# Kernel tuning notes

Measured on AMD Instinct MI355X. Metric: run time of the kernel, lower is better.

The kernel has to match this reference:

```python
import jax, jax.numpy as jnp
import numpy as np

INPUT_DIM = 256
RNN_DIM = 256
T, B = 1024, 64


def setup_inputs() -> dict:
    key = jax.random.key(0)
    ks = jax.random.split(key, 12)
    stdv = 1.0 / np.sqrt(RNN_DIM)
    u = lambda k, shape: jax.random.uniform(k, shape, jnp.float32, -stdv, stdv)
    return {
        "input_vectors": jax.random.normal(ks[0], (T, B, INPUT_DIM), jnp.float32),
        "W": u(ks[1], (INPUT_DIM, RNN_DIM)),
        "U": u(ks[2], (RNN_DIM, RNN_DIM)),
        "b": u(ks[3], (1, RNN_DIM)),
        "W_r": u(ks[4], (INPUT_DIM, RNN_DIM)),
        "U_r": u(ks[5], (RNN_DIM, RNN_DIM)),
        "b_r": u(ks[6], (1, RNN_DIM)),
        "W_z": u(ks[7], (INPUT_DIM, RNN_DIM)),
        "U_z": u(ks[8], (RNN_DIM, RNN_DIM)),
        "b_z": u(ks[9], (1, RNN_DIM)),
        "init_hidden": u(ks[10], (1, RNN_DIM)),
    }


def reference(input_vectors, W, U, b, W_r, U_r, b_r, W_z, U_z, b_z, init_hidden):
    # direction='l'. NOTE: the original module appends prev_hidden BEFORE the
    # update, so output[t] is the hidden state entering step t (output[0] is
    # the learned init). Also note the (nonstandard) combine uses (1-r), not
    # (1-z) \u2014 replicated faithfully.
    batch = input_vectors.shape[1]
    h0 = jnp.broadcast_to(init_hidden, (batch, RNN_DIM))

    def step(h, x):  # x: [B, input_dim], h: [B, rnn_dim]
        z = jax.nn.sigmoid(x @ W_z + h @ U_z + b_z)
        r = jax.nn.sigmoid(x @ W_r + h @ U_r + b_r)
        h_bar = jnp.tanh(x @ W + (r * h) @ U + b)
        new_h = (1.0 - r) * h + z * h_bar
        return new_h, h  # emit pre-update hidden, matching the torch code

    _, seq_hidden = jax.lax.scan(step, h0, input_vectors)
    return seq_hidden  # [T, B, rnn_dim]
```

## Files before the change

### kernel.cpp

```cpp
#include <hip/hip_runtime.h>
#include <hip/hip_bf16.h>

typedef __bf16 bf16x8 __attribute__((ext_vector_type(8)));
typedef __bf16 bf16x4 __attribute__((ext_vector_type(4)));
typedef float  f32x4  __attribute__((ext_vector_type(4)));
typedef unsigned int u32x4 __attribute__((ext_vector_type(4)));

#define T_STEPS 1024
#define LOG2E 1.4426950408889634f

#define LDS_BARRIER() asm volatile("s_waitcnt lgkmcnt(0)\n\ts_barrier" ::: "memory")

__device__ __forceinline__ float fast_sigmoid(float x) {
  float e = __builtin_amdgcn_exp2f(x * -LOG2E);
  return __builtin_amdgcn_rcpf(1.f + e);
}
__device__ __forceinline__ float fast_tanh(float x) {
  float e = __builtin_amdgcn_exp2f(x * (2.f * LOG2E));
  return 1.f - 2.f * __builtin_amdgcn_rcpf(1.f + e);
}
__device__ __forceinline__ float bf_lo(unsigned int u) { return __uint_as_float(u << 16); }
__device__ __forceinline__ float bf_hi(unsigned int u) { return __uint_as_float(u & 0xFFFF0000u); }


__global__ __launch_bounds__(256) void prep_frags(
    const float* __restrict__ Wz, const float* __restrict__ Wr, const float* __restrict__ Wh,
    const float* __restrict__ Uz, const float* __restrict__ Ur, const float* __restrict__ Uh,
    __bf16* __restrict__ afrag)
{
  int idx  = blockIdx.x * 256 + threadIdx.x;
  int mat  = idx >> 16;
  int cb   = (idx >> 12) & 15;
  int kblk = (idx >> 9) & 7;
  int l    = (idx >> 3) & 63;
  int j    = idx & 7;
  int k    = kblk * 32 + (l >> 4) * 8 + j;
  int col  = cb * 16 + (l & 15);
  const float* s = (mat == 0) ? Wz : (mat == 1) ? Wr : (mat == 2) ? Wh
                 : (mat == 3) ? Uz : (mat == 4) ? Ur : Uh;
  afrag[idx] = (__bf16)s[k * 256 + col];
}

__global__ __launch_bounds__(256) void gemm_x(
    const float* __restrict__ x, const __bf16* __restrict__ afrag,
    const float* __restrict__ bz, const float* __restrict__ br, const float* __restrict__ bh,
    __bf16* __restrict__ gates)
{
  int t = blockIdx.x;
  int tid = threadIdx.x;
  int l = tid & 63, w = tid >> 6;
  int q = l >> 4, m15 = l & 15;

  bf16x8 bfr[4][8];
#pragma unroll
  for (int g = 0; g < 4; g++) {
    const float* xrow = x + ((size_t)t * 64 + g * 16 + m15) * 256 + q * 8;
#pragma unroll
    for (int kb = 0; kb < 8; kb++) {
      f32x4 lo = *(const f32x4*)(xrow + kb * 32);
      f32x4 hi = *(const f32x4*)(xrow + kb * 32 + 4);
      bf16x8 v;
#pragma unroll
      for (int j = 0; j < 4; j++) { v[j] = (__bf16)lo[j]; v[4 + j] = (__bf16)hi[j]; }
      bfr[g][kb] = v;
    }
  }

  const bf16x8* af = (const bf16x8*)afrag;
#pragma unroll 1
  for (int jj = 0; jj < 12; jj++) {
    int nt = w + 4 * jj;
    int mat = nt >> 4, cb = nt & 15;
    f32x4 acc[4];
#pragma unroll
    for (int g = 0; g < 4; g++) acc[g] = (f32x4){0.f, 0.f, 0.f, 0.f};
#pragma unroll
    for (int kb = 0; kb < 8; kb++) {
      bf16x8 a = af[(nt * 8 + kb) * 64 + l];
#pragma unroll
      for (int g = 0; g < 4; g++)
        acc[g] = __builtin_amdgcn_mfma_f32_16x16x32_bf16(a, bfr[g][kb], acc[g], 0, 0, 0);
    }
    const float* bias = (mat == 0) ? bz : (mat == 1) ? br : bh;
    float b4[4];
#pragma unroll
    for (int i = 0; i < 4; i++) b4[i] = bias[cb * 16 + q * 4 + i];
    int p = cb >> 1, c = cb & 1;
#pragma unroll
    for (int g = 0; g < 4; g++) {
      bf16x4 ov;
#pragma unroll
      for (int i = 0; i < 4; i++) ov[i] = (__bf16)(acc[g][i] + b4[i]);
      *(bf16x4*)(gates + ((size_t)t * 4 + g) * 12288 + ((mat * 8 + p) * 64 + l) * 8 + c * 4) = ov;
    }
  }
}

__global__ __launch_bounds__(512, 2) void gru_rec(
    const __bf16* __restrict__ afrag, const __bf16* __restrict__ gates,
    const float* __restrict__ h0, float* __restrict__ out)
{
  __shared__ bf16x8 hfrag[512];
  __shared__ bf16x8 rhfrag[512];
  int g = blockIdx.x;
  int tid = threadIdx.x;
  int l = tid & 63, w = tid >> 6;
  int q = l >> 4, m15 = l & 15;

  bf16x8 wz[2][8], wr[2][8], wu[2][8];
  const bf16x8* af = (const bf16x8*)afrag;
#pragma unroll
  for (int c = 0; c < 2; c++) {
    int cbg = 2 * w + c;
#pragma unroll
    for (int kb = 0; kb < 8; kb++) {
      wz[c][kb] = af[((3 * 16 + cbg) * 8 + kb) * 64 + l];
      wr[c][kb] = af[((4 * 16 + cbg) * 8 + kb) * 64 + l];
      wu[c][kb] = af[((5 * 16 + cbg) * 8 + kb) * 64 + l];
    }
  }

  float hreg[2][4];
#pragma unroll
  for (int c = 0; c < 2; c++)
#pragma unroll
    for (int i = 0; i < 4; i++)
      hreg[c][i] = h0[32 * w + 16 * c + 4 * q + i];

  {
    const float* hp = h0 + w * 32 + q * 8;
    bf16x8 hv;
#pragma unroll
    for (int j = 0; j < 8; j++) hv[j] = (__bf16)hp[j];
    hfrag[w * 64 + l] = hv;
  }
  LDS_BARRIER();

  int wr0 = w * 128 + (m15 + 16 * (0 + (q >> 1))) * 2 + (q & 1);
  int wr1 = w * 128 + (m15 + 16 * (2 + (q >> 1))) * 2 + (q & 1);
  bf16x4* hf4  = (bf16x4*)hfrag;
  bf16x4* rhf4 = (bf16x4*)rhfrag;

  const int GSTRIDE = 4 * 12288;
  const __bf16* gt_p = gates + (size_t)g * 12288;
  int go_z = ((0 * 8 + w) * 64 + l) * 8;
  int go_r = ((1 * 8 + w) * 64 + l) * 8;
  int go_h = ((2 * 8 + w) * 64 + l) * 8;
  const float* out_t = out;
  int oo = (g * 16 + m15) * 256 + 32 * w + 4 * q;

  u32x4 nzu = *(const u32x4*)(gt_p + go_z);
  u32x4 nru = *(const u32x4*)(gt_p + go_r);

#pragma unroll 1
  for (int t = 0; t < T_STEPS; t++) {
    u32x4 ghu = *(const u32x4*)(gt_p + go_h);

    {
      f32x4 o0 = {hreg[0][0], hreg[0][1], hreg[0][2], hreg[0][3]};
      f32x4 o1 = {hreg[1][0], hreg[1][1], hreg[1][2], hreg[1][3]};
      *(f32x4*)(out_t + oo)      = o0;
      *(f32x4*)(out_t + oo + 16) = o1;
      out_t += 64 * 256;
    }

    f32x4 az0 = {bf_lo(nzu.x), bf_hi(nzu.x), bf_lo(nzu.y), bf_hi(nzu.y)};
    f32x4 az1 = {bf_lo(nzu.z), bf_hi(nzu.z), bf_lo(nzu.w), bf_hi(nzu.w)};
    f32x4 ar0 = {bf_lo(nru.x), bf_hi(nru.x), bf_lo(nru.y), bf_hi(nru.y)};
    f32x4 ar1 = {bf_lo(nru.z), bf_hi(nru.z), bf_lo(nru.w), bf_hi(nru.w)};
#pragma unroll
    for (int kb = 0; kb < 8; kb++) {
      bf16x8 hb = hfrag[kb * 64 + l];
      az0 = __builtin_amdgcn_mfma_f32_16x16x32_bf16(wz[0][kb], hb, az0, 0, 0, 0);
      az1 = __builtin_amdgcn_mfma_f32_16x16x32_bf16(wz[1][kb], hb, az1, 0, 0, 0);
      ar0 = __builtin_amdgcn_mfma_f32_16x16x32_bf16(wr[0][kb], hb, ar0, 0, 0, 0);
      ar1 = __builtin_amdgcn_mfma_f32_16x16x32_bf16(wr[1][kb], hb, ar1, 0, 0, 0);
    }
    float rhf[2][4];
    bf16x4 zb0, zb1, rhb0, rhb1;
#pragma unroll
    for (int i = 0; i < 4; i++) {
      float z0 = fast_sigmoid(az0[i]);
      float z1 = fast_sigmoid(az1[i]);
      float r0 = fast_sigmoid(ar0[i]);
      float r1 = fast_sigmoid(ar1[i]);
      zb0[i] = (__bf16)z0; zb1[i] = (__bf16)z1;
      rhf[0][i] = r0 * hreg[0][i];
      rhf[1][i] = r1 * hreg[1][i];
      rhb0[i] = (__bf16)rhf[0][i];
      rhb1[i] = (__bf16)rhf[1][i];
    }
    rhf4[wr0] = rhb0;
    rhf4[wr1] = rhb1;

    const __bf16* gn_p = gt_p + ((t < T_STEPS - 1) ? GSTRIDE : 0);
    nzu = *(const u32x4*)(gn_p + go_z);
    nru = *(const u32x4*)(gn_p + go_r);
    gt_p = gn_p;
    LDS_BARRIER();

    f32x4 ah0 = {bf_lo(ghu.x), bf_hi(ghu.x), bf_lo(ghu.y), bf_hi(ghu.y)};
    f32x4 ah1 = {bf_lo(ghu.z), bf_hi(ghu.z), bf_lo(ghu.w), bf_hi(ghu.w)};
#pragma unroll
    for (int kb = 0; kb < 8; kb++) {
      bf16x8 rb = rhfrag[kb * 64 + l];
      ah0 = __builtin_amdgcn_mfma_f32_16x16x32_bf16(wu[0][kb], rb, ah0, 0, 0, 0);
      ah1 = __builtin_amdgcn_mfma_f32_16x16x32_bf16(wu[1][kb], rb, ah1, 0, 0, 0);
    }
    bf16x4 nh0, nh1;
#pragma unroll
    for (int i = 0; i < 4; i++) {
      float hb0 = fast_tanh(ah0[i]);
      float hb1 = fast_tanh(ah1[i]);
      float z0 = (float)zb0[i], z1 = (float)zb1[i];
      hreg[0][i] = (hreg[0][i] - rhf[0][i]) + z0 * hb0;
      hreg[1][i] = (hreg[1][i] - rhf[1][i]) + z1 * hb1;
      nh0[i] = (__bf16)hreg[0][i];
      nh1[i] = (__bf16)hreg[1][i];
    }
    hf4[wr0] = nh0;
    hf4[wr1] = nh1;
    LDS_BARRIER();
  }
}

extern "C" void kernel_launch(void* const* d_in, const int* in_sizes, int n_in,
                              void* d_out, int out_size, void* d_ws, size_t ws_size,
                              hipStream_t stream)
{
  const float* x  = (const float*)d_in[0];
  const float* Wh = (const float*)d_in[1];
  const float* Uh = (const float*)d_in[2];
  const float* bh = (const float*)d_in[3];
  const float* Wr = (const float*)d_in[4];
  const float* Ur = (const float*)d_in[5];
  const float* br = (const float*)d_in[6];
  const float* Wz = (const float*)d_in[7];
  const float* Uz = (const float*)d_in[8];
  const float* bz = (const float*)d_in[9];
  const float* h0 = (const float*)d_in[10];

  __bf16* afrag = (__bf16*)d_ws;
  __bf16* gates = (__bf16*)d_ws + 393216;
  if (ws_size < (size_t)(393216 + 50331648) * 2) return;

  prep_frags<<<1536, 256, 0, stream>>>(Wz, Wr, Wh, Uz, Ur, Uh, afrag);
  gemm_x<<<1024, 256, 0, stream>>>(x, afrag, bz, br, bh, gates);
  gru_rec<<<4, 512, 0, stream>>>(afrag, gates, h0, (float*)d_out);
}
```

Measured before the change: 1.831 ms.

## Split recurrent step across 16 waves with double-buffered hidden state

The recurrent kernel now runs 1024 threads per block, so each wave owns one 16-column tile instead of two. This halves the serial MFMA chain per wave in each timestep. The z-gate matmul is moved after the first barrier, where it runs interleaved with the candidate matmul, so only the r-gate sits on the critical path before the r*h exchange. The hidden state is double-buffered in LDS across an unrolled pair of steps, and the update is folded into an fma. The cost is more waves competing at each barrier and less latency hiding per wave.

```diff
diff --git a/kernel.cpp b/kernel.cpp
--- a/kernel.cpp
+++ b/kernel.cpp
@@ -4,12 +4,14 @@
 typedef __bf16 bf16x8 __attribute__((ext_vector_type(8)));
 typedef __bf16 bf16x4 __attribute__((ext_vector_type(4)));
 typedef float  f32x4  __attribute__((ext_vector_type(4)));
-typedef unsigned int u32x4 __attribute__((ext_vector_type(4)));
+typedef unsigned int u32x2 __attribute__((ext_vector_type(2)));
 
 #define T_STEPS 1024
 #define LOG2E 1.4426950408889634f
 
 #define LDS_BARRIER() asm volatile("s_waitcnt lgkmcnt(0)\n\ts_barrier" ::: "memory")
+
+#define MFMA(a, b, c) __builtin_amdgcn_mfma_f32_16x16x32_bf16((a), (b), (c), 0, 0, 0)
 
 __device__ __forceinline__ float fast_sigmoid(float x) {
   float e = __builtin_amdgcn_exp2f(x * -LOG2E);
@@ -79,7 +81,7 @@
       bf16x8 a = af[(nt * 8 + kb) * 64 + l];
 #pragma unroll
       for (int g = 0; g < 4; g++)
-        acc[g] = __builtin_amdgcn_mfma_f32_16x16x32_bf16(a, bfr[g][kb], acc[g], 0, 0, 0);
+        acc[g] = MFMA(a, bfr[g][kb], acc[g]);
     }
     const float* bias = (mat == 0) ? bz : (mat == 1) ? br : bh;
     float b4[4];
@@ -96,131 +98,137 @@
   }
 }
 
-__global__ __launch_bounds__(512, 2) void gru_rec(
+__global__ __launch_bounds__(1024, 1) void gru_rec(
     const __bf16* __restrict__ afrag, const __bf16* __restrict__ gates,
     const float* __restrict__ h0, float* __restrict__ out)
 {
-  __shared__ bf16x8 hfrag[512];
-  __shared__ bf16x8 rhfrag[512];
+  __shared__ bf16x8 hfA[512];
+  __shared__ bf16x8 hfB[512];
+  __shared__ bf16x8 rhf[512];
   int g = blockIdx.x;
   int tid = threadIdx.x;
   int l = tid & 63, w = tid >> 6;
   int q = l >> 4, m15 = l & 15;
 
-  bf16x8 wz[2][8], wr[2][8], wu[2][8];
+  bf16x8 wz_[8], wr_[8], wu_[8];
   const bf16x8* af = (const bf16x8*)afrag;
 #pragma unroll
-  for (int c = 0; c < 2; c++) {
-    int cbg = 2 * w + c;
-#pragma unroll
-    for (int kb = 0; kb < 8; kb++) {
-      wz[c][kb] = af[((3 * 16 + cbg) * 8 + kb) * 64 + l];
-      wr[c][kb] = af[((4 * 16 + cbg) * 8 + kb) * 64 + l];
-      wu[c][kb] = af[((5 * 16 + cbg) * 8 + kb) * 64 + l];
-    }
-  }
-
-  float hreg[2][4];
-#pragma unroll
-  for (int c = 0; c < 2; c++)
-#pragma unroll
-    for (int i = 0; i < 4; i++)
-      hreg[c][i] = h0[32 * w + 16 * c + 4 * q + i];
-
-  {
+  for (int kb = 0; kb < 8; kb++) {
+    wz_[kb] = af[((3 * 16 + w) * 8 + kb) * 64 + l];
+    wr_[kb] = af[((4 * 16 + w) * 8 + kb) * 64 + l];
+    wu_[kb] = af[((5 * 16 + w) * 8 + kb) * 64 + l];
+  }
+
+  f32x4 hreg;
+#pragma unroll
+  for (int i = 0; i < 4; i++) hreg[i] = h0[16 * w + 4 * q + i];
+
+  if (w < 8) {
     const float* hp = h0 + w * 32 + q * 8;
     bf16x8 hv;
 #pragma unroll
     for (int j = 0; j < 8; j++) hv[j] = (__bf16)hp[j];
-    hfrag[w * 64 + l] = hv;
+    hfA[w * 64 + l] = hv;
   }
   LDS_BARRIER();
 
-  int wr0 = w * 128 + (m15 + 16 * (0 + (q >> 1))) * 2 + (q & 1);
-  int wr1 = w * 128 + (m15 + 16 * (2 + (q >> 1))) * 2 + (q & 1);
-  bf16x4* hf4  = (bf16x4*)hfrag;
-  bf16x4* rhf4 = (bf16x4*)rhfrag;
+  int slot = (w >> 1) * 128 + (m15 + 16 * ((2 * w + (q >> 1)) & 3)) * 2 + (q & 1);
+  bf16x4* rh4 = (bf16x4*)rhf;
+  bf16x4* hA4 = (bf16x4*)hfA;
+  bf16x4* hB4 = (bf16x4*)hfB;
 
   const int GSTRIDE = 4 * 12288;
   const __bf16* gt_p = gates + (size_t)g * 12288;
-  int go_z = ((0 * 8 + w) * 64 + l) * 8;
-  int go_r = ((1 * 8 + w) * 64 + l) * 8;
-  int go_h = ((2 * 8 + w) * 64 + l) * 8;
+  int go_z = ((0 * 8 + (w >> 1)) * 64 + l) * 8 + (w & 1) * 4;
+  int go_r = ((1 * 8 + (w >> 1)) * 64 + l) * 8 + (w & 1) * 4;
+  int go_h = ((2 * 8 + (w >> 1)) * 64 + l) * 8 + (w & 1) * 4;
   const float* out_t = out;
-  int oo = (g * 16 + m15) * 256 + 32 * w + 4 * q;
-
-  u32x4 nzu = *(const u32x4*)(gt_p + go_z);
-  u32x4 nru = *(const u32x4*)(gt_p + go_r);
+  int oo = (g * 16 + m15) * 256 + 16 * w + 4 * q;
+
+  u32x2 gru = *(const u32x2*)(gt_p + go_r);
 
 #pragma unroll 1
-  for (int t = 0; t < T_STEPS; t++) {
-    u32x4 ghu = *(const u32x4*)(gt_p + go_h);
-
+  for (int t = 0; t < T_STEPS; t += 2) {
     {
-      f32x4 o0 = {hreg[0][0], hreg[0][1], hreg[0][2], hreg[0][3]};
-      f32x4 o1 = {hreg[1][0], hreg[1][1], hreg[1][2], hreg[1][3]};
-      *(f32x4*)(out_t + oo)      = o0;
-      *(f32x4*)(out_t + oo + 16) = o1;
+      u32x2 gzu = *(const u32x2*)(gt_p + go_z);
+      u32x2 ghu = *(const u32x2*)(gt_p + go_h);
+      *(f32x4*)(out_t + oo) = hreg;
       out_t += 64 * 256;
-    }
-
-    f32x4 az0 = {bf_lo(nzu.x), bf_hi(nzu.x), bf_lo(nzu.y), bf_hi(nzu.y)};
-    f32x4 az1 = {bf_lo(nzu.z), bf_hi(nzu.z), bf_lo(nzu.w), bf_hi(nzu.w)};
-    f32x4 ar0 = {bf_lo(nru.x), bf_hi(nru.x), bf_lo(nru.y), bf_hi(nru.y)};
-    f32x4 ar1 = {bf_lo(nru.z), bf_hi(nru.z), bf_lo(nru.w), bf_hi(nru.w)};
-#pragma unroll
-    for (int kb = 0; kb < 8; kb++) {
-      bf16x8 hb = hfrag[kb * 64 + l];
-      az0 = __builtin_amdgcn_mfma_f32_16x16x32_bf16(wz[0][kb], hb, az0, 0, 0, 0);
-      az1 = __builtin_amdgcn_mfma_f32_16x16x32_bf16(wz[1][kb], hb, az1, 0, 0, 0);
-      ar0 = __builtin_amdgcn_mfma_f32_16x16x32_bf16(wr[0][kb], hb, ar0, 0, 0, 0);
-      ar1 = __builtin_amdgcn_mfma_f32_16x16x32_bf16(wr[1][kb], hb, ar1, 0, 0, 0);
-    }
-    float rhf[2][4];
-    bf16x4 zb0, zb1, rhb0, rhb1;
-#pragma unroll
-    for (int i = 0; i < 4; i++) {
-      float z0 = fast_sigmoid(az0[i]);
-      float z1 = fast_sigmoid(az1[i]);
-      float r0 = fast_sigmoid(ar0[i]);
-      float r1 = fast_sigmoid(ar1[i]);
-      zb0[i] = (__bf16)z0; zb1[i] = (__bf16)z1;
-      rhf[0][i] = r0 * hreg[0][i];
-      rhf[1][i] = r1 * hreg[1][i];
-      rhb0[i] = (__bf16)rhf[0][i];
-      rhb1[i] = (__bf16)rhf[1][i];
-    }
-    rhf4[wr0] = rhb0;
-    rhf4[wr1] = rhb1;
-
-    const __bf16* gn_p = gt_p + ((t < T_STEPS - 1) ? GSTRIDE : 0);
-    nzu = *(const u32x4*)(gn_p + go_z);
-    nru = *(const u32x4*)(gn_p + go_r);
-    gt_p = gn_p;
-    LDS_BARRIER();
-
-    f32x4 ah0 = {bf_lo(ghu.x), bf_hi(ghu.x), bf_lo(ghu.y), bf_hi(ghu.y)};
-    f32x4 ah1 = {bf_lo(ghu.z), bf_hi(ghu.z), bf_lo(ghu.w), bf_hi(ghu.w)};
-#pragma unroll
-    for (int kb = 0; kb < 8; kb++) {
-      bf16x8 rb = rhfrag[kb * 64 + l];
-      ah0 = __builtin_amdgcn_mfma_f32_16x16x32_bf16(wu[0][kb], rb, ah0, 0, 0, 0);
-      ah1 = __builtin_amdgcn_mfma_f32_16x16x32_bf16(wu[1][kb], rb, ah1, 0, 0, 0);
-    }
-    bf16x4 nh0, nh1;
-#pragma unroll
-    for (int i = 0; i < 4; i++) {
-      float hb0 = fast_tanh(ah0[i]);
-      float hb1 = fast_tanh(ah1[i]);
-      float z0 = (float)zb0[i], z1 = (float)zb1[i];
-      hreg[0][i] = (hreg[0][i] - rhf[0][i]) + z0 * hb0;
-      hreg[1][i] = (hreg[1][i] - rhf[1][i]) + z1 * hb1;
-      nh0[i] = (__bf16)hreg[0][i];
-      nh1[i] = (__bf16)hreg[1][i];
-    }
-    hf4[wr0] = nh0;
-    hf4[wr1] = nh1;
-    LDS_BARRIER();
+
+      f32x4 ar = {bf_lo(gru.x), bf_hi(gru.x), bf_lo(gru.y), bf_hi(gru.y)};
+#pragma unroll
+      for (int kb = 0; kb < 8; kb++) ar = MFMA(wr_[kb], hfA[kb * 64 + l], ar);
+      f32x4 hd; bf16x4 rhb;
+#pragma unroll
+      for (int i = 0; i < 4; i++) {
+        float r = fast_sigmoid(ar[i]);
+        float rh = r * hreg[i];
+        hd[i] = hreg[i] - rh;
+        rhb[i] = (__bf16)rh;
+      }
+      rh4[slot] = rhb;
+      gt_p += GSTRIDE;
+      gru = *(const u32x2*)(gt_p + go_r);
+      LDS_BARRIER();
+
+      f32x4 ah = {bf_lo(ghu.x), bf_hi(ghu.x), bf_lo(ghu.y), bf_hi(ghu.y)};
+      f32x4 az = {bf_lo(gzu.x), bf_hi(gzu.x), bf_lo(gzu.y), bf_hi(gzu.y)};
+#pragma unroll
+      for (int kb = 0; kb < 8; kb++) {
+        az = MFMA(wz_[kb], hfA[kb * 64 + l], az);
+        ah = MFMA(wu_[kb], rhf[kb * 64 + l], ah);
+      }
+      bf16x4 nh;
+#pragma unroll
+      for (int i = 0; i < 4; i++) {
+        float z = fast_sigmoid(az[i]);
+        float hb = fast_tanh(ah[i]);
+        hreg[i] = fmaf(z, hb, hd[i]);
+        nh[i] = (__bf16)hreg[i];
+      }
+      hB4[slot] = nh;
+      LDS_BARRIER();
+    }
+    {
+      u32x2 gzu = *(const u32x2*)(gt_p + go_z);
+      u32x2 ghu = *(const u32x2*)(gt_p + go_h);
+      *(f32x4*)(out_t + oo) = hreg;
+      out_t += 64 * 256;
+
+      f32x4 ar = {bf_lo(gru.x), bf_hi(gru.x), bf_lo(gru.y), bf_hi(gru.y)};
+#pragma unroll
+      for (int kb = 0; kb < 8; kb++) ar = MFMA(wr_[kb], hfB[kb * 64 + l], ar);
+      f32x4 hd; bf16x4 rhb;
+#pragma unroll
+      for (int i = 0; i < 4; i++) {
+        float r = fast_sigmoid(ar[i]);
+        float rh = r * hreg[i];
+        hd[i] = hreg[i] - rh;
+        rhb[i] = (__bf16)rh;
+      }
+      rh4[slot] = rhb;
+      gt_p += (t + 2 < T_STEPS) ? GSTRIDE : 0;
+      gru = *(const u32x2*)(gt_p + go_r);
+      LDS_BARRIER();
+
+      f32x4 ah = {bf_lo(ghu.x), bf_hi(ghu.x), bf_lo(ghu.y), bf_hi(ghu.y)};
+      f32x4 az = {bf_lo(gzu.x), bf_hi(gzu.x), bf_lo(gzu.y), bf_hi(gzu.y)};
+#pragma unroll
+      for (int kb = 0; kb < 8; kb++) {
+        az = MFMA(wz_[kb], hfB[kb * 64 + l], az);
+        ah = MFMA(wu_[kb], rhf[kb * 64 + l], ah);
+      }
+      bf16x4 nh;
+#pragma unroll
+      for (int i = 0; i < 4; i++) {
+        float z = fast_sigmoid(az[i]);
+        float hb = fast_tanh(ah[i]);
+        hreg[i] = fmaf(z, hb, hd[i]);
+        nh[i] = (__bf16)hreg[i];
+      }
+      hA4[slot] = nh;
+      LDS_BARRIER();
+    }
   }
 }
 
@@ -246,5 +254,5 @@
 
   prep_frags<<<1536, 256, 0, stream>>>(Wz, Wr, Wh, Uz, Ur, Uh, afrag);
   gemm_x<<<1024, 256, 0, stream>>>(x, afrag, bz, br, bh, gates);
-  gru_rec<<<4, 512, 0, stream>>>(afrag, gates, h0, (float*)d_out);
-}
+  gru_rec<<<4, 1024, 0, stream>>>(afrag, gates, h0, (float*)d_out);
+}
```

Result: slower. 2.928 ms (+59.9%).
